# Kernel optimization log

Hardware: AMD Instinct MI355X
Metric: run time of the kernel (lower is better)

Reference implementation:

```python
import jax, jax.numpy as jnp
import numpy as np

B, S, F, D, K = 4096, 64, 8, 64, 16  # batch_size, seq_len, input_size, d_model, knns


def setup_inputs() -> dict:
    key = jax.random.key(0)
    ks = jax.random.split(key, 3)
    return {
        "x": jax.random.normal(ks[0], (B, S, F), jnp.float32),
        "W_emb": jax.random.normal(ks[1], (F, D), jnp.float32) / np.sqrt(F),
        "b_emb": jnp.zeros((D,), jnp.float32),
        "W_proj": jax.random.normal(ks[2], (D, F), jnp.float32) / np.sqrt(D),
        "b_proj": jnp.zeros((F,), jnp.float32),
    }


def reference(x, W_emb, b_emb, W_proj, b_proj):
    # enc_embedding
    x_enc = x @ W_emb + b_emb                       # [B,S,D]
    x_re = x_enc.reshape(B, S * D)                  # flatten per sample
    # batch self-similarity
    attn = jnp.einsum('bl,cl->bc', x_re, x_re) / np.sqrt(D * S)
    diag = jnp.eye(B, dtype=bool)
    attn = jnp.where(diag, -jnp.inf, attn)
    scores = jax.nn.softmax(attn, axis=-1)          # [B,B]
    # einsum('bd,bc->bd', x_re, scores) == x_re * scores.sum(-1)
    x_rec = x_re * jnp.sum(scores, axis=-1, keepdims=True)
    x_rec = x_rec.reshape(B, S, D)
    x_rec_proj = x_rec @ W_proj + b_proj            # [B,S,F]
    # top-k neighbor gather
    _, top_idx = jax.lax.top_k(scores, K)           # [B,K] int32
    gathered = x_rec_proj[top_idx]                  # [B,K,S,F]
    diff_1 = jnp.mean(jnp.diff(gathered, axis=1) ** 2)
    diff_2 = jnp.mean(jnp.diff(gathered, axis=2) ** 2)
    loss = jnp.mean((x_rec_proj - x) ** 2) + diff_1 + diff_2  # var == 2
    return loss, x_rec_proj
```

## Files before the change

kernel.cpp:

```cpp
#include <hip/hip_runtime.h>
#include <math.h>

#define NB 4096
#define NS 64
#define NF 8
#define ND 64
#define KL 512
#define NK 16

typedef _Float16 half8 __attribute__((ext_vector_type(8)));
typedef float    f32x4 __attribute__((ext_vector_type(4)));

#define GLD16(src, dst) \
  __builtin_amdgcn_global_load_lds((const __attribute__((address_space(1))) void*)(src), \
                                   (__attribute__((address_space(3))) void*)(dst), 16, 0, 0)

#define WAITVM(N) asm volatile("s_waitcnt vmcnt(" #N ")" ::: "memory")

__device__ __forceinline__ unsigned short f2bf_rne(float f) {
    unsigned v = __float_as_uint(f);
    return (unsigned short)((v + 0x7FFFu + ((v >> 16) & 1u)) >> 16);
}
__device__ __forceinline__ unsigned bf16key(float v, int col) {
    const unsigned u = f2bf_rne(v);
    const unsigned s = (u & 0x8000u) ? (~u & 0xFFFFu) : (u | 0x8000u);
    return (s << 12) | (unsigned)(4095 - col);
}

#define UPD2(M1, M2, K) { const unsigned k_ = (K); \
    if (k_ > M1) { M2 = M1; M1 = k_; } else if (k_ > M2) M2 = k_; }
#define MERGE2(M1, M2, OFF) { \
    const unsigned o1 = (unsigned)__shfl_xor((int)M1, OFF, 64); \
    const unsigned o2 = (unsigned)__shfl_xor((int)M2, OFF, 64); \
    const unsigned hi = M1 > o1 ? M1 : o1; \
    const unsigned lo = M1 > o1 ? o1 : M1; \
    const unsigned mx = M2 > o2 ? M2 : o2; \
    M1 = hi; M2 = lo > mx ? lo : mx; }

__device__ __forceinline__ float blk_reduce(float v, float* red) {
    #pragma unroll
    for (int o = 32; o > 0; o >>= 1) v += __shfl_down(v, o, 64);
    const int t = threadIdx.x;
    __syncthreads();
    if ((t & 63) == 0) red[t >> 6] = v;
    __syncthreads();
    float r = 0.f;
    if (t == 0) r = red[0] + red[1] + red[2] + red[3];
    return r;
}

__global__ __launch_bounds__(64) void consts_kernel(
    const float* __restrict__ Wemb, const float* __restrict__ bemb,
    const float* __restrict__ Wp, const float* __restrict__ bp,
    float* __restrict__ cst, double* __restrict__ acc)
{
    __shared__ float sWe[NF * ND];
    __shared__ float sWp[ND * NF];
    __shared__ float sbe[ND];
    __shared__ float sbp[NF];
    const int t = threadIdx.x;
    #pragma unroll
    for (int i = 0; i < 12; ++i) acc[t + i * 64] = 0.0;
    #pragma unroll
    for (int i = 0; i < 8; ++i) { sWe[t + i * 64] = Wemb[t + i * 64]; sWp[t + i * 64] = Wp[t + i * 64]; }
    sbe[t] = bemb[t];
    if (t < NF) sbp[t] = bp[t];
    __syncthreads();
    const int f = t >> 3, f2 = t & 7;
    float g = 0.f, m = 0.f;
    #pragma unroll
    for (int d = 0; d < ND; ++d) {
        g += sWe[f * ND + d] * sWe[f2 * ND + d];
        m += sWe[f * ND + d] * sWp[d * NF + f2];
    }
    cst[t] = g;
    cst[64 + t] = m;
    if (t < NF) {
        float uu = 0.f, cc = 0.f;
        #pragma unroll
        for (int d = 0; d < ND; ++d) {
            uu += sWe[t * ND + d] * sbe[d];
            cc += sbe[d] * sWp[d * NF + t];
        }
        cst[128 + t] = uu;
        cst[136 + t] = cc + sbp[t];
    }
}

__global__ __launch_bounds__(256) void prep_kernel(
    const float* __restrict__ x, const float* __restrict__ cst,
    _Float16* __restrict__ X16, _Float16* __restrict__ Y16,
    float* __restrict__ proj, float* __restrict__ r, double* __restrict__ acc)
{
    __shared__ float sG[64], sM[64], su[8], sc[8];
    __shared__ float red[4];
    const int t = threadIdx.x, lane = t & 63, w = t >> 6;
    if (t < 64) sG[t] = cst[t];
    else if (t < 128) sM[t - 64] = cst[t];
    else if (t < 136) su[t - 128] = cst[t];
    else if (t < 144) sc[t - 136] = cst[t];
    __syncthreads();
    const int b = blockIdx.x * 4 + w;
    const size_t base = (size_t)b * KL + lane * 8;
    const f32x4 x0 = *(const f32x4*)&x[base];
    const f32x4 x1 = *(const f32x4*)&x[base + 4];
    float xv[8] = {x0[0], x0[1], x0[2], x0[3], x1[0], x1[1], x1[2], x1[3]};
    float yv[8], pv[8];
    #pragma unroll
    for (int f2 = 0; f2 < 8; ++f2) { yv[f2] = 0.f; pv[f2] = sc[f2]; }
    #pragma unroll
    for (int f = 0; f < 8; ++f)
        #pragma unroll
        for (int f2 = 0; f2 < 8; ++f2) {
            yv[f2] += xv[f] * sG[f * 8 + f2];
            pv[f2] += xv[f] * sM[f * 8 + f2];
        }
    half8 hx, hy;
    #pragma unroll
    for (int j = 0; j < 8; ++j) { hx[j] = (_Float16)xv[j]; hy[j] = (_Float16)yv[j]; }
    *(half8*)&X16[base] = hx;
    *(half8*)&Y16[base] = hy;
    *(f32x4*)&proj[base] = (f32x4){pv[0], pv[1], pv[2], pv[3]};
    *(f32x4*)&proj[base + 4] = (f32x4){pv[4], pv[5], pv[6], pv[7]};
    float rv = 0.f;
    #pragma unroll
    for (int f = 0; f < 8; ++f) rv += xv[f] * su[f];
    #pragma unroll
    for (int o = 32; o > 0; o >>= 1) rv += __shfl_down(rv, o, 64);
    if (lane == 0) r[b] = rv;
    float s1 = 0.f;
    #pragma unroll
    for (int j = 0; j < 8; ++j) { const float d = pv[j] - xv[j]; s1 += d * d; }
    const float tot = blk_reduce(s1, red);
    if (t == 0) atomicAdd(&acc[(size_t)(blockIdx.x & 31) * 8], (double)tot);
}

__global__ __launch_bounds__(256) void attn_gemm_kernel(
    const _Float16* __restrict__ Xf, const _Float16* __restrict__ Yf,
    const float* __restrict__ rvec, unsigned* __restrict__ cand)
{
    __shared__ __align__(16) char smem_raw[49152];
    _Float16* smem = (_Float16*)smem_raw;

    const int t = threadIdx.x;
    const int lane = t & 63, wid = t >> 6;
    const int wr = wid >> 1, wc = wid & 1;

    const int bid0 = blockIdx.x;
    const int bid = (bid0 & 7) * 66 + (bid0 >> 3);

    int it = (int)((sqrtf(8.0f * (float)bid + 1.0f) - 1.0f) * 0.5f);
    while ((it + 1) * (it + 2) / 2 <= bid) ++it;
    while (it * (it + 1) / 2 > bid) --it;
    const int jt = bid - it * (it + 1) / 2;
    const int i0 = it * 128, j0 = jt * 128;

    f32x4 acc[4][4];
    #pragma unroll
    for (int m = 0; m < 4; ++m)
        #pragma unroll
        for (int n = 0; n < 4; ++n) acc[m][n] = (f32x4){0.f, 0.f, 0.f, 0.f};

    const int lrow = lane & 15, g = lane >> 4;
    const int ksw = (g ^ ((lrow >> 1) & 3)) * 8;

    const int c0 = t, c1 = t + 256;
    const int r0 = c0 >> 2, r1 = c1 >> 2;
    const int cs0 = ((c0 & 3) ^ ((r0 >> 1) & 3)) * 8;
    const int cs1 = ((c1 & 3) ^ ((r1 >> 1) & 3)) * 8;
    const _Float16* pa0 = Xf + (size_t)(i0 + r0) * KL + cs0;
    const _Float16* pa1 = Xf + (size_t)(i0 + r1) * KL + cs1;
    const _Float16* pb0 = Yf + (size_t)(j0 + r0) * KL + cs0;
    const _Float16* pb1 = Yf + (size_t)(j0 + r1) * KL + cs1;
    _Float16* d0 = smem + c0 * 8;
    _Float16* d1 = smem + c1 * 8;

#define STG(BUF, KH) { \
    GLD16(pa0 + (KH), d0 + (BUF) * 8192); \
    GLD16(pa1 + (KH), d1 + (BUF) * 8192); \
    GLD16(pb0 + (KH), d0 + (BUF) * 8192 + 4096); \
    GLD16(pb1 + (KH), d1 + (BUF) * 8192 + 4096); }

    const int roA = wr * 2048 + lrow * 32 + ksw;
    const int roB = wc * 2048 + lrow * 32 + ksw;

#define COMPUTE(BUF) { \
    const _Float16* sA = smem + (BUF) * 8192; \
    const _Float16* sB = sA + 4096; \
    half8 fa[4], fb[4]; \
    _Pragma("unroll") \
    for (int m = 0; m < 4; ++m) { \
        fa[m] = *(const half8*)&sA[roA + m * 512]; \
        fb[m] = *(const half8*)&sB[roB + m * 512]; \
    } \
    __builtin_amdgcn_s_setprio(1); \
    _Pragma("unroll") \
    for (int m = 0; m < 4; ++m) \
        _Pragma("unroll") \
        for (int n = 0; n < 4; ++n) \
            acc[m][n] = __builtin_amdgcn_mfma_f32_16x16x32_f16(fa[m], fb[n], acc[m][n], 0, 0, 0); \
    __builtin_amdgcn_s_setprio(0); }

    STG(0, 0); STG(1, 32);
    pa0 += 64; pa1 += 64; pb0 += 64; pb1 += 64;
    #pragma unroll 1
    for (int io = 0; io < 4; ++io) {
        WAITVM(4); __builtin_amdgcn_s_barrier(); STG(2, 0);  COMPUTE(0);
        WAITVM(4); __builtin_amdgcn_s_barrier(); STG(0, 32); COMPUTE(1);
        WAITVM(4); __builtin_amdgcn_s_barrier(); STG(1, 64); COMPUTE(2);
        pa0 += 96; pa1 += 96; pb0 += 96; pb1 += 96;
    }
    WAITVM(4); __builtin_amdgcn_s_barrier(); STG(2, 0);  COMPUTE(0);
    WAITVM(4); __builtin_amdgcn_s_barrier(); STG(0, 32); COMPUTE(1);
    WAITVM(4); __builtin_amdgcn_s_barrier(); COMPUTE(2);
    WAITVM(0); __builtin_amdgcn_s_barrier(); COMPUTE(0);
#undef STG
#undef COMPUTE

    float rj[4];
    #pragma unroll
    for (int n = 0; n < 4; ++n) rj[n] = rvec[j0 + wc * 64 + n * 16 + lrow];

    const int diag = (it == jt);

    #pragma unroll
    for (int m = 0; m < 4; ++m)
        #pragma unroll
        for (int rr = 0; rr < 4; ++rr) {
            const int i = i0 + wr * 64 + m * 16 + g * 4 + rr;
            unsigned m1 = 0u, m2 = 0u;
            #pragma unroll
            for (int n = 0; n < 4; ++n) {
                const int j = j0 + wc * 64 + n * 16 + lrow;
                unsigned key = bf16key(acc[m][n][rr] + rj[n], j);
                if (i == j) key = 0u;
                UPD2(m1, m2, key)
            }
            MERGE2(m1, m2, 1) MERGE2(m1, m2, 2) MERGE2(m1, m2, 4) MERGE2(m1, m2, 8)
            if (lrow == 0) {
                uint2 st; st.x = m1; st.y = m2;
                *(uint2*)(cand + (size_t)i * 128 + (size_t)(jt * 2 + wc) * 2) = st;
            }
        }

    if (!diag) {
        #pragma unroll
        for (int n = 0; n < 4; ++n) {
            const int j = j0 + wc * 64 + n * 16 + lrow;
            unsigned m1 = 0u, m2 = 0u;
            #pragma unroll
            for (int m = 0; m < 4; ++m) {
                const f32x4 riv = *(const f32x4*)&rvec[i0 + wr * 64 + m * 16 + g * 4];
                #pragma unroll
                for (int rr = 0; rr < 4; ++rr) {
                    const int i = i0 + wr * 64 + m * 16 + g * 4 + rr;
                    UPD2(m1, m2, bf16key(acc[m][n][rr] + riv[rr], i))
                }
            }
            MERGE2(m1, m2, 16) MERGE2(m1, m2, 32)
            if (g == 0) {
                uint2 st; st.x = m1; st.y = m2;
                *(uint2*)(cand + (size_t)j * 128 + (size_t)(it * 2 + wr) * 2) = st;
            }
        }
    }
}

__global__ __launch_bounds__(256) void topk_diffs_kernel(
    const unsigned* __restrict__ cand, const float* __restrict__ proj,
    double* __restrict__ acc)
{
    const int t = threadIdx.x, lane = t & 63, w = t >> 6;
    const int b = blockIdx.x * 4 + w;
    const uint2 kk = *(const uint2*)(cand + (size_t)b * 128 + lane * 2);
    unsigned k0 = kk.x, k1 = kk.y;

    float s1 = 0.f, s2 = 0.f;
    float prev[8];

    for (int k = 0; k < NK; ++k) {
        unsigned bv = k0 > k1 ? k0 : k1;
        #pragma unroll
        for (int o = 1; o <= 32; o <<= 1)
            bv = max(bv, (unsigned)__shfl_xor((int)bv, o, 64));
        const int idx = 4095 - (int)(bv & 0xFFFu);

        const float* pp = proj + (size_t)idx * 512 + lane * 8;
        const f32x4 a0 = *(const f32x4*)pp;
        const f32x4 a1 = *(const f32x4*)(pp + 4);
        float cur[8] = {a0[0], a0[1], a0[2], a0[3], a1[0], a1[1], a1[2], a1[3]};
        if (k) {
            #pragma unroll
            for (int j = 0; j < 8; ++j) { const float d = cur[j] - prev[j]; s1 += d * d; }
        }
        if (lane < 63) {
            const f32x4 n0 = *(const f32x4*)(pp + 8);
            const f32x4 n1 = *(const f32x4*)(pp + 12);
            const float nxt[8] = {n0[0], n0[1], n0[2], n0[3], n1[0], n1[1], n1[2], n1[3]};
            #pragma unroll
            for (int j = 0; j < 8; ++j) { const float d = nxt[j] - cur[j]; s2 += d * d; }
        }
        #pragma unroll
        for (int j = 0; j < 8; ++j) prev[j] = cur[j];

        if (k0 == bv) k0 = 0u;
        if (k1 == bv) k1 = 0u;
    }

    #pragma unroll
    for (int o = 32; o > 0; o >>= 1) { s1 += __shfl_down(s1, o, 64); s2 += __shfl_down(s2, o, 64); }
    if (lane == 0) {
        const size_t slot = (size_t)(blockIdx.x & 31) * 8;
        atomicAdd(&acc[(size_t)32 * 8 + slot], (double)s1);
        atomicAdd(&acc[(size_t)64 * 8 + slot], (double)s2);
    }
}

__global__ void finalize_kernel(const double* __restrict__ acc, float* __restrict__ out) {
    if (threadIdx.x == 0) {
        double s0 = 0.0, s1 = 0.0, s2 = 0.0;
        #pragma unroll
        for (int i = 0; i < 32; ++i) {
            s0 += acc[(size_t)i * 8];
            s1 += acc[(size_t)(32 + i) * 8];
            s2 += acc[(size_t)(64 + i) * 8];
        }
        out[0] = (float)(s0 / 2097152.0 + s1 / 31457280.0 + s2 / 33030144.0);
    }
}

extern "C" void kernel_launch(void* const* d_in, const int* in_sizes, int n_in,
                              void* d_out, int out_size, void* d_ws, size_t ws_size,
                              hipStream_t stream) {
    const float* x    = (const float*)d_in[0];
    const float* Wemb = (const float*)d_in[1];
    const float* bemb = (const float*)d_in[2];
    const float* Wp   = (const float*)d_in[3];
    const float* bp   = (const float*)d_in[4];
    float* out  = (float*)d_out;
    float* proj = out + 1;

    char* ws = (char*)d_ws;
    _Float16* X16 = (_Float16*)ws;
    _Float16* Y16 = (_Float16*)(ws + ((size_t)4 << 20));
    unsigned* cand = (unsigned*)(ws + ((size_t)8 << 20));
    float*  cst   = (float*)(ws + ((size_t)10 << 20));
    float*  rvec  = (float*)(ws + ((size_t)10 << 20) + 4096);
    double* acc   = (double*)(ws + ((size_t)10 << 20) + 65536);

    consts_kernel<<<1, 64, 0, stream>>>(Wemb, bemb, Wp, bp, cst, acc);
    prep_kernel<<<NB / 4, 256, 0, stream>>>(x, cst, X16, Y16, proj, rvec, acc);
    attn_gemm_kernel<<<(32 * 33) / 2, 256, 0, stream>>>(X16, Y16, rvec, cand);
    topk_diffs_kernel<<<NB / 4, 256, 0, stream>>>(cand, proj, acc);
    finalize_kernel<<<1, 64, 0, stream>>>(acc, out);
}
```

Baseline: 72.43 us.

## Stage GEMM tile through LDS for per-row top-2 instead of shuffle merges

Replaces the cross-lane shuffle-based top-2 merging in the epilogue of the similarity GEMM with a transpose through LDS. Each half of the tile is written to shared memory and 128 threads then scan a full row or column serially to find the top-2 keys. This removes many shfl_xor merge steps but adds barriers and serialized phases in which only half the threads work, using swizzled and padded layouts to avoid bank conflicts.

```diff
diff --git a/kernel.cpp b/kernel.cpp
--- a/kernel.cpp
+++ b/kernel.cpp
@@ -29,13 +29,6 @@
 
 #define UPD2(M1, M2, K) { const unsigned k_ = (K); \
     if (k_ > M1) { M2 = M1; M1 = k_; } else if (k_ > M2) M2 = k_; }
-#define MERGE2(M1, M2, OFF) { \
-    const unsigned o1 = (unsigned)__shfl_xor((int)M1, OFF, 64); \
-    const unsigned o2 = (unsigned)__shfl_xor((int)M2, OFF, 64); \
-    const unsigned hi = M1 > o1 ? M1 : o1; \
-    const unsigned lo = M1 > o1 ? o1 : M1; \
-    const unsigned mx = M2 > o2 ? M2 : o2; \
-    M1 = hi; M2 = lo > mx ? lo : mx; }
 
 __device__ __forceinline__ float blk_reduce(float v, float* red) {
     #pragma unroll
@@ -217,50 +210,73 @@
 #undef STG
 #undef COMPUTE
 
+    float* lds = (float*)smem_raw;
+    const int diag = (it == jt);
+
     float rj[4];
     #pragma unroll
     for (int n = 0; n < 4; ++n) rj[n] = rvec[j0 + wc * 64 + n * 16 + lrow];
 
-    const int diag = (it == jt);
-
-    #pragma unroll
-    for (int m = 0; m < 4; ++m)
-        #pragma unroll
-        for (int rr = 0; rr < 4; ++rr) {
-            const int i = i0 + wr * 64 + m * 16 + g * 4 + rr;
+    #pragma unroll 1
+    for (int p = 0; p < 2; ++p) {
+        __syncthreads();
+        if (wc == p) {
+            #pragma unroll
+            for (int m = 0; m < 4; ++m)
+                #pragma unroll
+                for (int n = 0; n < 4; ++n) {
+                    const int cl = n * 16 + lrow;
+                    const int rw = wr * 64 + m * 16 + g * 4;
+                    f32x4 v = acc[m][n];
+                    v[0] += rj[n]; v[1] += rj[n]; v[2] += rj[n]; v[3] += rj[n];
+                    if (diag) {
+                        #pragma unroll
+                        for (int rr = 0; rr < 4; ++rr)
+                            if (rw + rr == p * 64 + cl) v[rr] = -INFINITY;
+                    }
+                    *(f32x4*)&lds[cl * 132 + rw] = v;
+                }
+        }
+        __syncthreads();
+        if (t < 128) {
             unsigned m1 = 0u, m2 = 0u;
-            #pragma unroll
-            for (int n = 0; n < 4; ++n) {
-                const int j = j0 + wc * 64 + n * 16 + lrow;
-                unsigned key = bf16key(acc[m][n][rr] + rj[n], j);
-                if (i == j) key = 0u;
-                UPD2(m1, m2, key)
+            #pragma unroll 8
+            for (int c = 0; c < 64; ++c) {
+                UPD2(m1, m2, bf16key(lds[c * 132 + t], j0 + p * 64 + c))
             }
-            MERGE2(m1, m2, 1) MERGE2(m1, m2, 2) MERGE2(m1, m2, 4) MERGE2(m1, m2, 8)
-            if (lrow == 0) {
-                uint2 st; st.x = m1; st.y = m2;
-                *(uint2*)(cand + (size_t)i * 128 + (size_t)(jt * 2 + wc) * 2) = st;
-            }
-        }
+            uint2 st; st.x = m1; st.y = m2;
+            *(uint2*)(cand + (size_t)(i0 + t) * 128 + (size_t)(jt * 2 + p) * 2) = st;
+        }
+    }
 
     if (!diag) {
-        #pragma unroll
-        for (int n = 0; n < 4; ++n) {
-            const int j = j0 + wc * 64 + n * 16 + lrow;
-            unsigned m1 = 0u, m2 = 0u;
-            #pragma unroll
-            for (int m = 0; m < 4; ++m) {
-                const f32x4 riv = *(const f32x4*)&rvec[i0 + wr * 64 + m * 16 + g * 4];
+        #pragma unroll 1
+        for (int q = 0; q < 2; ++q) {
+            __syncthreads();
+            if (wr == q) {
                 #pragma unroll
-                for (int rr = 0; rr < 4; ++rr) {
-                    const int i = i0 + wr * 64 + m * 16 + g * 4 + rr;
-                    UPD2(m1, m2, bf16key(acc[m][n][rr] + riv[rr], i))
+                for (int m = 0; m < 4; ++m) {
+                    const f32x4 riv = *(const f32x4*)&rvec[i0 + q * 64 + m * 16 + g * 4];
+                    #pragma unroll
+                    for (int n = 0; n < 4; ++n) {
+                        const int col = wc * 64 + n * 16 + lrow;
+                        const int chunk = (m * 4 + g) ^ (col & 15);
+                        f32x4 v = acc[m][n];
+                        v[0] += riv[0]; v[1] += riv[1]; v[2] += riv[2]; v[3] += riv[3];
+                        *(f32x4*)&lds[col * 64 + chunk * 4] = v;
+                    }
                 }
             }
-            MERGE2(m1, m2, 16) MERGE2(m1, m2, 32)
-            if (g == 0) {
+            __syncthreads();
+            if (t < 128) {
+                unsigned m1 = 0u, m2 = 0u;
+                #pragma unroll 8
+                for (int rr2 = 0; rr2 < 64; ++rr2) {
+                    const int ad = t * 64 + (((rr2 >> 2) ^ (t & 15)) << 2) + (rr2 & 3);
+                    UPD2(m1, m2, bf16key(lds[ad], i0 + q * 64 + rr2))
+                }
                 uint2 st; st.x = m1; st.y = m2;
-                *(uint2*)(cand + (size_t)j * 128 + (size_t)(it * 2 + wr) * 2) = st;
+                *(uint2*)(cand + (size_t)(j0 + t) * 128 + (size_t)(it * 2 + q) * 2) = st;
             }
         }
     }
```

Result: slower. 91.80 us (+26.7%).
